# Performance work log

Measured on AMD Instinct MI355X. Metric: run time of the kernel, lower is better.

Reference implementation:

```python
import jax, jax.numpy as jnp
import numpy as np

B, D, MAXC = 16384, 64, 8
NPROB, NCON, TDIM, HID = 50000, 2000, 1024, 256

def setup_inputs() -> dict:
    key = jax.random.key(0)
    ks = jax.random.split(key, 20)
    s = 0.02
    return {
        'prob_ids': jax.random.randint(ks[0], (B,), 0, NPROB),
        'related_concept_index': jax.random.randint(ks[1], (B, MAXC), 0, NCON),
        'filter0': jax.random.randint(ks[2], (B, MAXC), 0, 2),
        'h': jax.random.normal(ks[3], (B, D), jnp.float32),
        'emb': jax.random.normal(ks[4], (B, 2 * D), jnp.float32),
        'operate': jax.random.randint(ks[5], (B, 1), 0, 2).astype(jnp.float32),
        'exercise_text_emb': jax.random.normal(ks[6], (NPROB, TDIM), jnp.float32) * s,
        'concept_text_emb': jax.random.normal(ks[7], (NCON, TDIM), jnp.float32) * s,
        'W1': jax.random.normal(ks[8], (TDIM, HID), jnp.float32) * s,
        'b1': jnp.zeros((HID,), jnp.float32),
        'W2': jax.random.normal(ks[9], (HID, D), jnp.float32) * s,
        'b2': jnp.zeros((D,), jnp.float32),
        'Wp': jax.random.normal(ks[10], (5 * D, 1), jnp.float32) * s,
        'bp': jnp.zeros((1,), jnp.float32),
        'Wx': jax.random.normal(ks[11], (4 * D, 3 * D), jnp.float32) * s,
        'Wh': jax.random.normal(ks[12], (D, 3 * D), jnp.float32) * s,
        'bx': jnp.zeros((3 * D,), jnp.float32),
        'bh': jnp.zeros((3 * D,), jnp.float32),
    }

def reference(prob_ids, related_concept_index, filter0, h, emb, operate,
              exercise_text_emb, concept_text_emb,
              W1, b1, W2, b2, Wp, bp, Wx, Wh, bx, bh):
    def text_proj(x):  # 1024 -> 256 -> 64 (dropout off at inference)
        return jax.nn.relu(x @ W1 + b1) @ W2 + b2

    red_prob = text_proj(exercise_text_emb)      # [NPROB, D]
    red_con = text_proj(concept_text_emb)        # [NCON, D]

    related = red_con[related_concept_index]     # gather: [B, MAXC, D]

    # text weights: cosine similarity of raw BERT embs (torch eps=1e-8)
    q = exercise_text_emb[prob_ids]              # [B, 1024]
    c = concept_text_emb[related_concept_index]  # [B, MAXC, 1024]
    dot = jnp.einsum('bd,bmd->bm', q, c)
    qn = jnp.sqrt(jnp.sum(q * q, axis=-1))[:, None]
    cn = jnp.sqrt(jnp.sum(c * c, axis=-1))
    tw = dot / jnp.maximum(qn * cn, 1e-8)
    tw = jnp.where(filter0 == 0, jnp.float32(-1e9), tw)
    tw = jax.nn.softmax(tw, axis=1)              # [B, MAXC]

    rep = jnp.einsum('bmd,bm->bd', related, tw)  # weighted concept sum
    v = jnp.concatenate([red_prob[prob_ids], rep], axis=1)  # [B, 2D]

    # predictor: funcs(n_layer=1, dim*5, 1) ~ single Linear
    prob = jnp.concatenate([h, v, emb], axis=1) @ Wp + bp   # [B, 1]

    # update_state -> GRU cell (mygru: input 4D, hidden D)
    op = operate
    v_cat = jnp.concatenate([v * op, v * (1 - op)], axis=1)
    e_cat = jnp.concatenate([emb * (1 - op), emb * op], axis=1)
    x = v_cat + e_cat                             # [B, 4D]
    xg = x @ Wx + bx
    hg = h @ Wh + bh
    xr, xz, xn = jnp.split(xg, 3, axis=1)
    hr, hz, hn = jnp.split(hg, 3, axis=1)
    r = jax.nn.sigmoid(xr + hr)
    z = jax.nn.sigmoid(xz + hz)
    n = jnp.tanh(xn + r * hn)
    h_next = (1 - z) * n + z * h                  # [B, D]
    return (prob, h_next)
```

## Files before the change

### kernel.cpp

```cpp
#include <hip/hip_runtime.h>
#include <cstdint>
#include <cstddef>

typedef unsigned short u16;
typedef unsigned char u8;
typedef long long i64;
typedef unsigned long long u64;
typedef __bf16 bf16x8 __attribute__((ext_vector_type(8)));
typedef float f32x4 __attribute__((ext_vector_type(4)));
typedef float f32x2 __attribute__((ext_vector_type(2)));
typedef u16 u16x4 __attribute__((ext_vector_type(4)));
typedef u16 u16x8 __attribute__((ext_vector_type(8)));

#define B_ 16384
#define D_ 64
#define MAXC_ 8
#define NCON_ 2000
#define NCONP_ 2048
#define TDIM_ 1024
#define HID_ 256

#define VMW(n) asm volatile("s_waitcnt vmcnt(" #n ")" ::: "memory")
#define BAR() __builtin_amdgcn_s_barrier()

__device__ inline u16 f2b(float f){
  unsigned u = __float_as_uint(f);
  u += 0x7fffu + ((u >> 16) & 1u);
  return (u16)(u >> 16);
}
__device__ inline float b2f(u16 u){ return __uint_as_float(((unsigned)u) << 16); }

__device__ inline unsigned pk2fp8(float a, float b){
  return (unsigned)__builtin_amdgcn_cvt_pk_fp8_f32(a, b, 0, false);
}

__device__ inline void gload16(const void* g, void* l){
  __builtin_amdgcn_global_load_lds((const __attribute__((address_space(1))) unsigned*)g,
                                   (__attribute__((address_space(3))) unsigned*)l, 16, 0, 0);
}

__device__ inline float wsum(float v){
  #pragma unroll
  for (int o = 32; o; o >>= 1) v += __shfl_xor(v, o);
  return v;
}
__device__ inline float sigf(float x){ return 1.f / (1.f + __expf(-x)); }

__global__ __launch_bounds__(256) void k_prep(
    const float* __restrict__ ex, const int* __restrict__ pid,
    const float* __restrict__ con,
    const float* __restrict__ W1, const float* __restrict__ W2,
    const float* __restrict__ Wx, const float* __restrict__ Wh,
    const float* __restrict__ bx, const float* __restrict__ bh,
    u8* __restrict__ qb8, float* __restrict__ qn,
    u8* __restrict__ cb8, float* __restrict__ cn,
    u8* __restrict__ W1T8, u16* __restrict__ W2T, u16* __restrict__ WxhT,
    float* __restrict__ bxh)
{
  const int bid = blockIdx.x, tid = threadIdx.x;
  const int lane = tid & 63;
  if (bid < 4096){
    const int b = bid * 4 + (tid >> 6);
    const float* src = ex + (size_t)pid[b] * TDIM_;
    u8* dst8 = qb8 + (size_t)b * TDIM_;
    float ss = 0.f;
    #pragma unroll
    for (int c = 0; c < 4; ++c){
      float4 v = *(const float4*)(src + c * 256 + lane * 4);
      ss += v.x*v.x + v.y*v.y + v.z*v.z + v.w*v.w;
      unsigned lo = pk2fp8(v.x * 32.f, v.y * 32.f);
      unsigned hi = pk2fp8(v.z * 32.f, v.w * 32.f);
      *(unsigned*)(dst8 + c * 256 + lane * 4) = (lo & 0xffffu) | (hi << 16);
    }
    ss = wsum(ss);
    if (lane == 0) qn[b] = sqrtf(ss);
  } else if (bid < 4608){
    const int r = (bid - 4096) * 4 + (tid >> 6);
    u8* dst8 = cb8 + (size_t)r * TDIM_;
    if (r < NCON_){
      const float* src = con + (size_t)r * TDIM_;
      float ss = 0.f;
      #pragma unroll
      for (int c = 0; c < 4; ++c){
        float4 v = *(const float4*)(src + c * 256 + lane * 4);
        ss += v.x*v.x + v.y*v.y + v.z*v.z + v.w*v.w;
        unsigned lo = pk2fp8(v.x * 32.f, v.y * 32.f);
        unsigned hi = pk2fp8(v.z * 32.f, v.w * 32.f);
        *(unsigned*)(dst8 + c * 256 + lane * 4) = (lo & 0xffffu) | (hi << 16);
      }
      ss = wsum(ss);
      if (lane == 0) cn[r] = sqrtf(ss);
    } else {
      #pragma unroll
      for (int c = 0; c < 4; ++c)
        *(unsigned*)(dst8 + c * 256 + lane * 4) = 0u;
    }
  } else {
    int gid = (bid - 4608) * 256 + tid;
    if (gid < 131072){
      int n = gid >> 9, k2 = (gid & 511) * 2;
      unsigned pk = pk2fp8(W1[(size_t)k2 * 256 + n] * 32.f,
                           W1[(size_t)(k2 + 1) * 256 + n] * 32.f);
      *(u16*)(W1T8 + (size_t)n * 1024 + k2) = (u16)pk;
    } else if (gid < 147456){
      int t = gid - 131072;
      int n = t >> 8, k = t & 255;
      W2T[t] = f2b(W2[(size_t)k * 64 + n]);
    } else if (gid < 229376){
      int t = gid - 147456;
      int c = t / 320, k = t % 320;
      int g = (c >> 4) & 3;
      int d = (c >> 6) * 16 + (c & 15);
      float v = 0.f;
      if (k < 256){
        if (g == 0)      v = Wx[(size_t)k * 192 + d];
        else if (g == 1) v = Wx[(size_t)k * 192 + 64 + d];
        else if (g == 2) v = Wx[(size_t)k * 192 + 128 + d];
      } else {
        int kh = k - 256;
        if (g == 0)      v = Wh[(size_t)kh * 192 + d];
        else if (g == 1) v = Wh[(size_t)kh * 192 + 64 + d];
        else if (g == 3) v = Wh[(size_t)kh * 192 + 128 + d];
      }
      WxhT[t] = f2b(v);
    } else if (gid < 229632){
      int c = gid - 229376;
      int g = (c >> 4) & 3;
      int d = (c >> 6) * 16 + (c & 15);
      float v;
      if (g == 0)      v = bx[d] + bh[d];
      else if (g == 1) v = bx[64 + d] + bh[64 + d];
      else if (g == 2) v = bx[128 + d];
      else             v = bh[128 + d];
      bxh[c] = v;
    }
  }
}

__global__ __launch_bounds__(512) void k_mlp(
    const u8* __restrict__ qb8, const u8* __restrict__ cb8,
    const u8* __restrict__ W1T8, const float* __restrict__ b1,
    const u16* __restrict__ W2T, const float* __restrict__ b2,
    float* __restrict__ redq, float* __restrict__ redc)
{
  __shared__ char SMm[53248];
  u16* Hs = (u16*)(SMm + 36864);
  const int tid = threadIdx.x;
  const int lane = tid & 63;
  const int w = tid >> 6;
  const int lr = lane & 15, lq = lane >> 4;
  const bool qside = blockIdx.x < 512;
  const u8* Abase = qside ? qb8 : cb8;
  float* Obase = qside ? redq : redc;
  const int m0 = (qside ? (int)blockIdx.x : ((int)blockIdx.x - 512)) << 5;
  const int rf = w & 1, ch = w >> 1;

  auto stage = [&](int buf, int kt){
    u8* Ab = (u8*)SMm + buf * 18432;
    u8* Bb = Ab + 2048;
    #pragma unroll
    for (int i = 0; i < 2; ++i){
      int e = i * 512 + tid;
      int slot = e >> 2, q4 = e & 3;
      int sw = (slot ^ (slot >> 2)) & 3;
      gload16(W1T8 + (size_t)slot * 1024 + kt * 64 + ((q4 ^ sw) << 4), Bb + e * 16);
    }
    if (tid < 128){
      int slot = tid >> 2, q4 = tid & 3;
      int sw = (slot ^ (slot >> 2)) & 3;
      gload16(Abase + (size_t)(m0 + slot) * TDIM_ + kt * 64 + ((q4 ^ sw) << 4),
              Ab + tid * 16);
    }
  };

  f32x4 acc[4] = {};
  stage(0, 0);
  int buf = 0;
  for (int kt = 0; kt < 16; ++kt){
    if (kt < 15){
      stage(buf ^ 1, kt + 1);
      if (w < 2) VMW(3); else VMW(2);
    } else VMW(0);
    BAR();
    const u8* Ab = (const u8*)SMm + buf * 18432;
    const u8* Bb = Ab + 2048;
    #pragma unroll
    for (int ks = 0; ks < 2; ++ks){
      const int h8 = ks * 4 + lq;
      const int arow = rf * 16 + lr;
      const int asw = (arow ^ (arow >> 2)) & 3;
      i64 a = *(const i64*)(Ab + arow * 64 + (((h8 >> 1) ^ asw) << 4) + (h8 & 1) * 8);
      #pragma unroll
      for (int fc = 0; fc < 4; ++fc){
        int brow = ch * 64 + fc * 16 + lr;
        int bsw = (brow ^ (brow >> 2)) & 3;
        i64 bv = *(const i64*)(Bb + brow * 64 + (((h8 >> 1) ^ bsw) << 4) + (h8 & 1) * 8);
        acc[fc] = __builtin_amdgcn_mfma_f32_16x16x32_fp8_fp8(a, bv, acc[fc], 0, 0, 0);
      }
    }
    BAR();
    buf ^= 1;
  }
  #pragma unroll
  for (int fc = 0; fc < 4; ++fc){
    int col = ch * 64 + fc * 16 + lr;
    float bv = b1[col];
    #pragma unroll
    for (int j = 0; j < 4; ++j){
      int rr = rf * 16 + lq * 4 + j;
      float v = fmaxf(acc[fc][j] * (1.f / 1024.f) + bv, 0.f);
      *(u16*)((char*)Hs + rr * 512 + ((col * 2) ^ ((rr & 7) << 4))) = f2b(v);
    }
  }
  __syncthreads();
  const int rf2 = w & 1, cp = w >> 1;
  f32x4 acc2 = {};
  #pragma unroll
  for (int ks2 = 0; ks2 < 8; ++ks2){
    int rr = rf2 * 16 + lr;
    int kb2 = ks2 * 64 + lq * 16;
    bf16x8 af2 = *(const bf16x8*)((const char*)Hs + rr * 512 + (kb2 ^ ((rr & 7) << 4)));
    bf16x8 w2 = *(const bf16x8*)(W2T + (size_t)(cp * 16 + lr) * 256 + ks2 * 32 + lq * 8);
    acc2 = __builtin_amdgcn_mfma_f32_16x16x32_bf16(af2, w2, acc2, 0, 0, 0);
  }
  {
    int col = cp * 16 + lr;
    float bv = b2[col];
    #pragma unroll
    for (int j = 0; j < 4; ++j){
      int rr = m0 + rf2 * 16 + lq * 4 + j;
      Obase[(size_t)rr * 64 + col] = acc2[j] + bv;
    }
  }
}

__global__ __launch_bounds__(512) void k_mixgru(
    const u8* __restrict__ qb8, const u8* __restrict__ cb8,
    const float* __restrict__ qn, const float* __restrict__ cn,
    const int* __restrict__ rci, const int* __restrict__ filt,
    const float* __restrict__ redq, const float* __restrict__ redc,
    const float* __restrict__ h, const float* __restrict__ emb,
    const float* __restrict__ op, const float* __restrict__ Wp,
    const float* __restrict__ bp, const u16* __restrict__ WxhT,
    const float* __restrict__ bxh, float* __restrict__ prob_out,
    float* __restrict__ outh)
{
  __shared__ char SM[67584];
  u8*    QsF  = (u8*)SM;
  u16*   XH   = (u16*)SM;
  float* DOTS = (float*)(SM + 20480);
  int*   SIDX = (int*)(SM + 32768);
  int*   SFLT = (int*)(SM + 33792);
  u8*    CsB  = (u8*)(SM + 34816);
  u16*   Bs   = (u16*)(SM + 34816);
  const int tid = threadIdx.x;
  const int lane = tid & 63;
  const int w = tid >> 6;
  const int m0 = blockIdx.x << 5;

  #pragma unroll
  for (int i = 0; i < 4; ++i){
    int e = i * 512 + tid;
    int row = e >> 6, c16 = e & 63;
    gload16(qb8 + (size_t)(m0 + row) * TDIM_ + ((c16 ^ (row & 7)) << 4),
            QsF + e * 16);
  }
  if (tid < 256) SIDX[tid] = rci[m0 * MAXC_ + tid];
  else           SFLT[tid - 256] = filt[m0 * MAXC_ + (tid - 256)];
  __syncthreads();

  auto stageC = [&](int buf, int kt){
    #pragma unroll
    for (int i = 0; i < 2; ++i){
      int e = i * 512 + tid;
      int slot = e >> 2, q4 = e & 3;
      int sw = (slot ^ (slot >> 2)) & 3;
      gload16(cb8 + (size_t)SIDX[slot] * TDIM_ + kt * 64 + ((q4 ^ sw) << 4),
              CsB + buf * 16384 + e * 16);
    }
  };

  const int R = w >> 2;
  const int cc0 = (w & 3) * 2;
  f32x4 dacc[2] = {};
  stageC(0, 0);
  int bufc = 0;
  for (int kt = 0; kt < 16; ++kt){
    if (kt < 15){ stageC(bufc ^ 1, kt + 1); VMW(2); }
    else        { VMW(0); }
    BAR();
    const u8* Cs = CsB + bufc * 16384;
    #pragma unroll
    for (int ks = 0; ks < 2; ++ks){
      const int h8 = ks * 4 + (lane >> 4);
      const int arow = R * 16 + (lane & 15);
      const int c16r = kt * 4 + (h8 >> 1);
      i64 a = *(const i64*)(QsF + arow * 1024 + ((c16r ^ (arow & 7)) << 4) + (h8 & 1) * 8);
      #pragma unroll
      for (int t = 0; t < 2; ++t){
        int slot = (R * 8 + cc0 + t) * 16 + (lane & 15);
        int bsw = (slot ^ (slot >> 2)) & 3;
        i64 bfr = *(const i64*)(Cs + slot * 64 + (((h8 >> 1) ^ bsw) << 4) + (h8 & 1) * 8);
        dacc[t] = __builtin_amdgcn_mfma_f32_16x16x32_fp8_fp8(a, bfr, dacc[t], 0, 0, 0);
      }
    }
    BAR();
    bufc ^= 1;
  }
  #pragma unroll
  for (int t = 0; t < 2; ++t){
    const int cc = cc0 + t;
    const int col = lane & 15;
    #pragma unroll
    for (int j = 0; j < 4; ++j){
      int tr = (lane >> 4) * 4 + j;
      if (tr == 2 * cc && col < 8)       DOTS[(R * 16 + tr) * 8 + col] = dacc[t][j];
      if (tr == 2 * cc + 1 && col >= 8)  DOTS[(R * 16 + tr) * 8 + col - 8] = dacc[t][j];
    }
  }
  auto stageB = [&](int kt){
    #pragma unroll
    for (int i = 0; i < 4; ++i){
      int cc = i * 512 + tid;
      int r2 = cc >> 3, s2 = cc & 7;
      gload16(WxhT + (size_t)r2 * 320 + kt * 64 + ((s2 ^ (r2 & 7)) << 3), &Bs[cc * 8]);
    }
  };
  __syncthreads();
  stageB(0);

  for (int i = 0; i < 4; ++i){
    const int r = w * 4 + i;
    const int b = m0 + r;
    int idxm[MAXC_];
    #pragma unroll
    for (int m = 0; m < MAXC_; ++m) idxm[m] = SIDX[r * MAXC_ + m];
    const float qnb = qn[b];
    float sv[MAXC_]; float mx = -3.0e38f;
    #pragma unroll
    for (int m = 0; m < MAXC_; ++m){
      float dnm = fmaxf(qnb * cn[idxm[m]], 1e-8f);
      float s = (SFLT[r * MAXC_ + m] == 0) ? -1e9f
              : DOTS[r * 8 + m] * (1.f / 1024.f) / dnm;
      sv[m] = s; mx = fmaxf(mx, s);
    }
    float se = 0.f;
    #pragma unroll
    for (int m = 0; m < MAXC_; ++m){ sv[m] = __expf(sv[m] - mx); se += sv[m]; }
    const float inv = 1.f / se;
    float rep = 0.f;
    #pragma unroll
    for (int m = 0; m < MAXC_; ++m) rep += sv[m] * redc[(size_t)idxm[m] * D_ + lane];
    rep *= inv;
    const float v0 = redq[(size_t)b * D_ + lane];
    const float hv = h[(size_t)b * D_ + lane];
    const float e0 = emb[(size_t)b * 128 + lane];
    const float e1 = emb[(size_t)b * 128 + 64 + lane];
    float p = hv * Wp[lane] + v0 * Wp[64 + lane] + rep * Wp[128 + lane]
            + e0 * Wp[192 + lane] + e1 * Wp[256 + lane];
    p = wsum(p);
    if (lane == 0) prob_out[b] = p + bp[0];
    const float o = op[b], om = 1.f - o;
    auto xst = [&](int col, float v){
      *(u16*)((char*)XH + r * 640 + ((col * 2) ^ ((r & 7) << 4))) = f2b(v);
    };
    xst(lane,        v0 * o  + e0 * om);
    xst(64 + lane,   rep * o + e1 * om);
    xst(128 + lane,  v0 * om + e0 * o);
    xst(192 + lane,  rep * om + e1 * o);
    xst(256 + lane,  hv);
  }
  __syncthreads();

  const int lr = lane & 15, lq = lane >> 4;
  const int rh = w & 1, cc2 = w >> 1;
  f32x4 acc[4] = {};
  for (int kt = 0; kt < 5; ++kt){
    VMW(0);
    BAR();
    #pragma unroll
    for (int ks = 0; ks < 2; ++ks){
      const int kb = ks * 64 + lq * 16;
      int rra = rh * 16 + lr;
      bf16x8 af = *(const bf16x8*)((const char*)XH + rra * 640 +
                                   ((kt * 128 + kb) ^ ((rra & 7) << 4)));
      bf16x8 bfr[4];
      #pragma unroll
      for (int fc = 0; fc < 4; ++fc){
        int rr = cc2 * 64 + fc * 16 + lr;
        bfr[fc] = *(const bf16x8*)((const char*)Bs + rr * 128 + (kb ^ ((rr & 7) << 4)));
      }
      #pragma unroll
      for (int fc = 0; fc < 4; ++fc)
        acc[fc] = __builtin_amdgcn_mfma_f32_16x16x32_bf16(af, bfr[fc], acc[fc], 0, 0, 0);
    }
    BAR();
    if (kt < 4) stageB(kt + 1);
  }
  const int d = cc2 * 16 + lr;
  float bg[4];
  #pragma unroll
  for (int g = 0; g < 4; ++g) bg[g] = bxh[cc2 * 64 + g * 16 + lr];
  #pragma unroll
  for (int j = 0; j < 4; ++j){
    float rv = sigf(acc[0][j] + bg[0]);
    float zv = sigf(acc[1][j] + bg[1]);
    float nv = tanhf(acc[2][j] + bg[2] + rv * (acc[3][j] + bg[3]));
    int rr = m0 + rh * 16 + lq * 4 + j;
    float hv = h[(size_t)rr * 64 + d];
    outh[(size_t)rr * 64 + d] = (1.f - zv) * nv + zv * hv;
  }
}

extern "C" void kernel_launch(void* const* d_in, const int* in_sizes, int n_in,
                              void* d_out, int out_size, void* d_ws, size_t ws_size,
                              hipStream_t stream) {
  const int*   prob_ids = (const int*)  d_in[0];
  const int*   rci      = (const int*)  d_in[1];
  const int*   filt     = (const int*)  d_in[2];
  const float* h        = (const float*)d_in[3];
  const float* emb      = (const float*)d_in[4];
  const float* op       = (const float*)d_in[5];
  const float* ex       = (const float*)d_in[6];
  const float* con      = (const float*)d_in[7];
  const float* W1       = (const float*)d_in[8];
  const float* b1       = (const float*)d_in[9];
  const float* W2       = (const float*)d_in[10];
  const float* b2       = (const float*)d_in[11];
  const float* Wp       = (const float*)d_in[12];
  const float* bp       = (const float*)d_in[13];
  const float* Wx       = (const float*)d_in[14];
  const float* Wh       = (const float*)d_in[15];
  const float* bx       = (const float*)d_in[16];
  const float* bh       = (const float*)d_in[17];
  float* out = (float*)d_out;

  char* w = (char*)d_ws;
  size_t off = 0;
  auto alloc = [&](size_t bytes){ size_t o = off; off = (off + bytes + 255) & ~(size_t)255; return o; };
  u8*    qb8  = (u8*)   (w + alloc((size_t)B_ * TDIM_));
  u8*    cb8  = (u8*)   (w + alloc((size_t)NCONP_ * TDIM_));
  float* qn   = (float*)(w + alloc((size_t)B_ * 4));
  float* cn   = (float*)(w + alloc((size_t)NCONP_ * 4));
  float* redq = (float*)(w + alloc((size_t)B_ * D_ * 4));
  float* redc = (float*)(w + alloc((size_t)NCONP_ * D_ * 4));
  u8*    W1T8 = (u8*)   (w + alloc((size_t)HID_ * TDIM_));
  u16*   W2T  = (u16*)  (w + alloc((size_t)D_ * HID_ * 2));
  u16*   WxhT = (u16*)  (w + alloc((size_t)256 * 320 * 2));
  float* bxh  = (float*)(w + alloc((size_t)256 * 4));

  k_prep<<<5505, 256, 0, stream>>>(ex, prob_ids, con, W1, W2, Wx, Wh, bx, bh,
                                   qb8, qn, cb8, cn, W1T8, W2T, WxhT, bxh);
  k_mlp<<<576, 512, 0, stream>>>(qb8, cb8, W1T8, b1, W2T, b2, redq, redc);
  k_mixgru<<<512, 512, 0, stream>>>(qb8, cb8, qn, cn, rci, filt, redq, redc,
                                    h, emb, op, Wp, bp, WxhT, bxh, out, out + B_);
}
```

Before: 71.59 us.

## Fuse query-side text MLP into mix/GRU kernel, keep projection in LDS

The query-side 1024->256->64 projection moves out of the separate MLP kernel and into the mix/GRU kernel. It reuses the query fp8 tile already staged in shared memory and keeps the reduced vector in LDS instead of writing it to global memory and reading it back. The MLP kernel now handles only the concept table with 64 blocks. This removes one global round trip of the query projection and its separate reload of the query rows, at the cost of a longer fused kernel with more shared memory and a serialized W1 phase before the cosine/dot phase.

```diff
diff --git a/kernel.cpp b/kernel.cpp
--- a/kernel.cpp
+++ b/kernel.cpp
@@ -9,7 +9,6 @@
 typedef __bf16 bf16x8 __attribute__((ext_vector_type(8)));
 typedef float f32x4 __attribute__((ext_vector_type(4)));
 typedef float f32x2 __attribute__((ext_vector_type(2)));
-typedef u16 u16x4 __attribute__((ext_vector_type(4)));
 typedef u16 u16x8 __attribute__((ext_vector_type(8)));
 
 #define B_ 16384
@@ -137,11 +136,11 @@
   }
 }
 
-__global__ __launch_bounds__(512) void k_mlp(
-    const u8* __restrict__ qb8, const u8* __restrict__ cb8,
+__global__ __launch_bounds__(512) void k_cmlp(
+    const u8* __restrict__ cb8,
     const u8* __restrict__ W1T8, const float* __restrict__ b1,
     const u16* __restrict__ W2T, const float* __restrict__ b2,
-    float* __restrict__ redq, float* __restrict__ redc)
+    float* __restrict__ redc)
 {
   __shared__ char SMm[53248];
   u16* Hs = (u16*)(SMm + 36864);
@@ -149,10 +148,7 @@
   const int lane = tid & 63;
   const int w = tid >> 6;
   const int lr = lane & 15, lq = lane >> 4;
-  const bool qside = blockIdx.x < 512;
-  const u8* Abase = qside ? qb8 : cb8;
-  float* Obase = qside ? redq : redc;
-  const int m0 = (qside ? (int)blockIdx.x : ((int)blockIdx.x - 512)) << 5;
+  const int m0 = (int)blockIdx.x << 5;
   const int rf = w & 1, ch = w >> 1;
 
   auto stage = [&](int buf, int kt){
@@ -168,7 +164,7 @@
     if (tid < 128){
       int slot = tid >> 2, q4 = tid & 3;
       int sw = (slot ^ (slot >> 2)) & 3;
-      gload16(Abase + (size_t)(m0 + slot) * TDIM_ + kt * 64 + ((q4 ^ sw) << 4),
+      gload16(cb8 + (size_t)(m0 + slot) * TDIM_ + kt * 64 + ((q4 ^ sw) << 4),
               Ab + tid * 16);
     }
   };
@@ -229,33 +225,37 @@
     #pragma unroll
     for (int j = 0; j < 4; ++j){
       int rr = m0 + rf2 * 16 + lq * 4 + j;
-      Obase[(size_t)rr * 64 + col] = acc2[j] + bv;
-    }
-  }
-}
-
-__global__ __launch_bounds__(512) void k_mixgru(
+      redc[(size_t)rr * 64 + col] = acc2[j] + bv;
+    }
+  }
+}
+
+__global__ __launch_bounds__(512, 4) void k_fused(
     const u8* __restrict__ qb8, const u8* __restrict__ cb8,
     const float* __restrict__ qn, const float* __restrict__ cn,
     const int* __restrict__ rci, const int* __restrict__ filt,
-    const float* __restrict__ redq, const float* __restrict__ redc,
+    const float* __restrict__ redc,
     const float* __restrict__ h, const float* __restrict__ emb,
     const float* __restrict__ op, const float* __restrict__ Wp,
-    const float* __restrict__ bp, const u16* __restrict__ WxhT,
-    const float* __restrict__ bxh, float* __restrict__ prob_out,
-    float* __restrict__ outh)
+    const float* __restrict__ bp,
+    const u8* __restrict__ W1T8, const float* __restrict__ b1,
+    const u16* __restrict__ W2T, const float* __restrict__ b2,
+    const u16* __restrict__ WxhT, const float* __restrict__ bxh,
+    float* __restrict__ prob_out, float* __restrict__ outh)
 {
-  __shared__ char SM[67584];
+  __shared__ char SM[75776];
   u8*    QsF  = (u8*)SM;
   u16*   XH   = (u16*)SM;
   float* DOTS = (float*)(SM + 20480);
-  int*   SIDX = (int*)(SM + 32768);
-  int*   SFLT = (int*)(SM + 33792);
-  u8*    CsB  = (u8*)(SM + 34816);
-  u16*   Bs   = (u16*)(SM + 34816);
+  u16*   Hs   = (u16*)(SM + 32768);
+  u16*   Bs   = (u16*)(SM + 32768);
+  float* Rq   = (float*)(SM + 65536);
+  int*   SIDX = (int*)(SM + 73728);
+  int*   SFLT = (int*)(SM + 74752);
   const int tid = threadIdx.x;
   const int lane = tid & 63;
   const int w = tid >> 6;
+  const int lr = lane & 15, lq = lane >> 4;
   const int m0 = blockIdx.x << 5;
 
   #pragma unroll
@@ -265,47 +265,120 @@
     gload16(qb8 + (size_t)(m0 + row) * TDIM_ + ((c16 ^ (row & 7)) << 4),
             QsF + e * 16);
   }
-  if (tid < 256) SIDX[tid] = rci[m0 * MAXC_ + tid];
-  else           SFLT[tid - 256] = filt[m0 * MAXC_ + (tid - 256)];
-  __syncthreads();
-
+  int rv;
+  if (tid < 256) rv = rci[m0 * MAXC_ + tid];
+  else           rv = filt[m0 * MAXC_ + (tid - 256)];
+
+  auto stageW1 = [&](int buf, int kt){
+    u8* Bb = (u8*)SM + 32768 + buf * 16384;
+    #pragma unroll
+    for (int i = 0; i < 2; ++i){
+      int e = i * 512 + tid;
+      int slot = e >> 2, q4 = e & 3;
+      int sw = (slot ^ (slot >> 2)) & 3;
+      gload16(W1T8 + (size_t)slot * 1024 + kt * 64 + ((q4 ^ sw) << 4), Bb + e * 16);
+    }
+  };
   auto stageC = [&](int buf, int kt){
+    u8* Bb = (u8*)SM + 32768 + buf * 16384;
     #pragma unroll
     for (int i = 0; i < 2; ++i){
       int e = i * 512 + tid;
       int slot = e >> 2, q4 = e & 3;
       int sw = (slot ^ (slot >> 2)) & 3;
       gload16(cb8 + (size_t)SIDX[slot] * TDIM_ + kt * 64 + ((q4 ^ sw) << 4),
-              CsB + buf * 16384 + e * 16);
+              Bb + e * 16);
     }
   };
+
+  const int rf = w & 1, ch = w >> 1;
+  f32x4 acc[4] = {};
+  stageW1(0, 0);
+  int buf = 0;
+  for (int kt = 0; kt < 16; ++kt){
+    if (kt < 15){ stageW1(buf ^ 1, kt + 1); VMW(2); }
+    else        { VMW(0); }
+    BAR();
+    const u8* Bb = (const u8*)SM + 32768 + buf * 16384;
+    #pragma unroll
+    for (int ks = 0; ks < 2; ++ks){
+      const int h8 = ks * 4 + lq;
+      const int arow = rf * 16 + lr;
+      const int c16r = kt * 4 + (h8 >> 1);
+      i64 a = *(const i64*)(QsF + arow * 1024 + ((c16r ^ (arow & 7)) << 4) + (h8 & 1) * 8);
+      #pragma unroll
+      for (int fc = 0; fc < 4; ++fc){
+        int brow = ch * 64 + fc * 16 + lr;
+        int bsw = (brow ^ (brow >> 2)) & 3;
+        i64 bv = *(const i64*)(Bb + brow * 64 + (((h8 >> 1) ^ bsw) << 4) + (h8 & 1) * 8);
+        acc[fc] = __builtin_amdgcn_mfma_f32_16x16x32_fp8_fp8(a, bv, acc[fc], 0, 0, 0);
+      }
+    }
+    BAR();
+    buf ^= 1;
+  }
+  #pragma unroll
+  for (int fc = 0; fc < 4; ++fc){
+    int col = ch * 64 + fc * 16 + lr;
+    float bv = b1[col];
+    #pragma unroll
+    for (int j = 0; j < 4; ++j){
+      int rr = rf * 16 + lq * 4 + j;
+      float v = fmaxf(acc[fc][j] * (1.f / 1024.f) + bv, 0.f);
+      *(u16*)((char*)Hs + rr * 512 + ((col * 2) ^ ((rr & 7) << 4))) = f2b(v);
+    }
+  }
+  if (tid < 256) SIDX[tid] = rv;
+  else           SFLT[tid - 256] = rv;
+  __syncthreads();
+
+  stageC(1, 0);
+  {
+    const int rf2 = w & 1, cp = w >> 1;
+    f32x4 acc2 = {};
+    #pragma unroll
+    for (int ks2 = 0; ks2 < 8; ++ks2){
+      int rr = rf2 * 16 + lr;
+      int kb2 = ks2 * 64 + lq * 16;
+      bf16x8 af2 = *(const bf16x8*)((const char*)Hs + rr * 512 + (kb2 ^ ((rr & 7) << 4)));
+      bf16x8 w2 = *(const bf16x8*)(W2T + (size_t)(cp * 16 + lr) * 256 + ks2 * 32 + lq * 8);
+      acc2 = __builtin_amdgcn_mfma_f32_16x16x32_bf16(af2, w2, acc2, 0, 0, 0);
+    }
+    int col = cp * 16 + lr;
+    float bv = b2[col];
+    #pragma unroll
+    for (int j = 0; j < 4; ++j){
+      int rr = rf2 * 16 + lq * 4 + j;
+      Rq[rr * 64 + col] = acc2[j] + bv;
+    }
+  }
+  __syncthreads();
 
   const int R = w >> 2;
   const int cc0 = (w & 3) * 2;
   f32x4 dacc[2] = {};
-  stageC(0, 0);
-  int bufc = 0;
+  int bufd = 1;
   for (int kt = 0; kt < 16; ++kt){
-    if (kt < 15){ stageC(bufc ^ 1, kt + 1); VMW(2); }
+    if (kt < 15){ stageC(bufd ^ 1, kt + 1); VMW(2); }
     else        { VMW(0); }
     BAR();
-    const u8* Cs = CsB + bufc * 16384;
+    const u8* Cs = (const u8*)SM + 32768 + bufd * 16384;
     #pragma unroll
     for (int ks = 0; ks < 2; ++ks){
-      const int h8 = ks * 4 + (lane >> 4);
-      const int arow = R * 16 + (lane & 15);
+      const int h8 = ks * 4 + lq;
+      const int arow = R * 16 + lr;
       const int c16r = kt * 4 + (h8 >> 1);
       i64 a = *(const i64*)(QsF + arow * 1024 + ((c16r ^ (arow & 7)) << 4) + (h8 & 1) * 8);
       #pragma unroll
       for (int t = 0; t < 2; ++t){
-        int slot = (R * 8 + cc0 + t) * 16 + (lane & 15);
+        int slot = (R * 8 + cc0 + t) * 16 + lr;
         int bsw = (slot ^ (slot >> 2)) & 3;
         i64 bfr = *(const i64*)(Cs + slot * 64 + (((h8 >> 1) ^ bsw) << 4) + (h8 & 1) * 8);
         dacc[t] = __builtin_amdgcn_mfma_f32_16x16x32_fp8_fp8(a, bfr, dacc[t], 0, 0, 0);
       }
     }
     BAR();
-    bufc ^= 1;
+    bufd ^= 1;
   }
   #pragma unroll
   for (int t = 0; t < 2; ++t){
@@ -313,7 +386,7 @@
     const int col = lane & 15;
     #pragma unroll
     for (int j = 0; j < 4; ++j){
-      int tr = (lane >> 4) * 4 + j;
+      int tr = lq * 4 + j;
       if (tr == 2 * cc && col < 8)       DOTS[(R * 16 + tr) * 8 + col] = dacc[t][j];
       if (tr == 2 * cc + 1 && col >= 8)  DOTS[(R * 16 + tr) * 8 + col - 8] = dacc[t][j];
     }
@@ -352,7 +425,7 @@
     #pragma unroll
     for (int m = 0; m < MAXC_; ++m) rep += sv[m] * redc[(size_t)idxm[m] * D_ + lane];
     rep *= inv;
-    const float v0 = redq[(size_t)b * D_ + lane];
+    const float v0 = Rq[r * 64 + lane];
     const float hv = h[(size_t)b * D_ + lane];
     const float e0 = emb[(size_t)b * 128 + lane];
     const float e1 = emb[(size_t)b * 128 + 64 + lane];
@@ -372,9 +445,8 @@
   }
   __syncthreads();
 
-  const int lr = lane & 15, lq = lane >> 4;
   const int rh = w & 1, cc2 = w >> 1;
-  f32x4 acc[4] = {};
+  f32x4 gacc[4] = {};
   for (int kt = 0; kt < 5; ++kt){
     VMW(0);
     BAR();
@@ -392,7 +464,7 @@
       }
       #pragma unroll
       for (int fc = 0; fc < 4; ++fc)
-        acc[fc] = __builtin_amdgcn_mfma_f32_16x16x32_bf16(af, bfr[fc], acc[fc], 0, 0, 0);
+        gacc[fc] = __builtin_amdgcn_mfma_f32_16x16x32_bf16(af, bfr[fc], gacc[fc], 0, 0, 0);
     }
     BAR();
     if (kt < 4) stageB(kt + 1);
@@ -403,9 +475,9 @@
   for (int g = 0; g < 4; ++g) bg[g] = bxh[cc2 * 64 + g * 16 + lr];
   #pragma unroll
   for (int j = 0; j < 4; ++j){
-    float rv = sigf(acc[0][j] + bg[0]);
-    float zv = sigf(acc[1][j] + bg[1]);
-    float nv = tanhf(acc[2][j] + bg[2] + rv * (acc[3][j] + bg[3]));
+    float rvv = sigf(gacc[0][j] + bg[0]);
+    float zv = sigf(gacc[1][j] + bg[1]);
+    float nv = tanhf(gacc[2][j] + bg[2] + rvv * (gacc[3][j] + bg[3]));
     int rr = m0 + rh * 16 + lq * 4 + j;
     float hv = h[(size_t)rr * 64 + d];
     outh[(size_t)rr * 64 + d] = (1.f - zv) * nv + zv * hv;
@@ -442,7 +514,6 @@
   u8*    cb8  = (u8*)   (w + alloc((size_t)NCONP_ * TDIM_));
   float* qn   = (float*)(w + alloc((size_t)B_ * 4));
   float* cn   = (float*)(w + alloc((size_t)NCONP_ * 4));
-  float* redq = (float*)(w + alloc((size_t)B_ * D_ * 4));
   float* redc = (float*)(w + alloc((size_t)NCONP_ * D_ * 4));
   u8*    W1T8 = (u8*)   (w + alloc((size_t)HID_ * TDIM_));
   u16*   W2T  = (u16*)  (w + alloc((size_t)D_ * HID_ * 2));
@@ -451,7 +522,8 @@
 
   k_prep<<<5505, 256, 0, stream>>>(ex, prob_ids, con, W1, W2, Wx, Wh, bx, bh,
                                    qb8, qn, cb8, cn, W1T8, W2T, WxhT, bxh);
-  k_mlp<<<576, 512, 0, stream>>>(qb8, cb8, W1T8, b1, W2T, b2, redq, redc);
-  k_mixgru<<<512, 512, 0, stream>>>(qb8, cb8, qn, cn, rci, filt, redq, redc,
-                                    h, emb, op, Wp, bp, WxhT, bxh, out, out + B_);
-}
+  k_cmlp<<<64, 512, 0, stream>>>(cb8, W1T8, b1, W2T, b2, redc);
+  k_fused<<<512, 512, 0, stream>>>(qb8, cb8, qn, cn, rci, filt, redc,
+                                   h, emb, op, Wp, bp,
+                                   W1T8, b1, W2T, b2, WxhT, bxh, out, out + B_);
+}
```

Measured after the change: 72.15 us. About the same (+0.8%).

## Compute cosine text weights in query-prep kernel using fp32 query and fp8 concepts

Applied to the files above, without the earlier changes.

Splits the prep kernel into a concept/weight prep kernel and a query prep kernel. The query kernel now also computes the dot products against the gathered fp8 concept rows, using the fp32 query values already in registers, and writes the softmaxed text weights to a buffer. This removes the fp8 MFMA dot-product stage, its LDS staging and the qn buffer from the GRU kernel, which then just reads the weights. The cost is an extra kernel launch, a serial dependency of query prep on concept prep, and scalar gathered loads in place of MFMA for the dots.

```diff
diff --git a/kernel.cpp b/kernel.cpp
--- a/kernel.cpp
+++ b/kernel.cpp
@@ -9,7 +9,6 @@
 typedef __bf16 bf16x8 __attribute__((ext_vector_type(8)));
 typedef float f32x4 __attribute__((ext_vector_type(4)));
 typedef float f32x2 __attribute__((ext_vector_type(2)));
-typedef u16 u16x4 __attribute__((ext_vector_type(4)));
 typedef u16 u16x8 __attribute__((ext_vector_type(8)));
 
 #define B_ 16384
@@ -33,6 +32,10 @@
 __device__ inline unsigned pk2fp8(float a, float b){
   return (unsigned)__builtin_amdgcn_cvt_pk_fp8_f32(a, b, 0, false);
 }
+template<bool HI>
+__device__ inline f32x2 unpk_fp8(unsigned v){
+  return __builtin_amdgcn_cvt_pk_f32_fp8(v, HI);
+}
 
 __device__ inline void gload16(const void* g, void* l){
   __builtin_amdgcn_global_load_lds((const __attribute__((address_space(1))) unsigned*)g,
@@ -46,36 +49,19 @@
 }
 __device__ inline float sigf(float x){ return 1.f / (1.f + __expf(-x)); }
 
-__global__ __launch_bounds__(256) void k_prep(
-    const float* __restrict__ ex, const int* __restrict__ pid,
+__global__ __launch_bounds__(256) void k_prepc(
     const float* __restrict__ con,
     const float* __restrict__ W1, const float* __restrict__ W2,
     const float* __restrict__ Wx, const float* __restrict__ Wh,
     const float* __restrict__ bx, const float* __restrict__ bh,
-    u8* __restrict__ qb8, float* __restrict__ qn,
     u8* __restrict__ cb8, float* __restrict__ cn,
     u8* __restrict__ W1T8, u16* __restrict__ W2T, u16* __restrict__ WxhT,
     float* __restrict__ bxh)
 {
   const int bid = blockIdx.x, tid = threadIdx.x;
   const int lane = tid & 63;
-  if (bid < 4096){
-    const int b = bid * 4 + (tid >> 6);
-    const float* src = ex + (size_t)pid[b] * TDIM_;
-    u8* dst8 = qb8 + (size_t)b * TDIM_;
-    float ss = 0.f;
-    #pragma unroll
-    for (int c = 0; c < 4; ++c){
-      float4 v = *(const float4*)(src + c * 256 + lane * 4);
-      ss += v.x*v.x + v.y*v.y + v.z*v.z + v.w*v.w;
-      unsigned lo = pk2fp8(v.x * 32.f, v.y * 32.f);
-      unsigned hi = pk2fp8(v.z * 32.f, v.w * 32.f);
-      *(unsigned*)(dst8 + c * 256 + lane * 4) = (lo & 0xffffu) | (hi << 16);
-    }
-    ss = wsum(ss);
-    if (lane == 0) qn[b] = sqrtf(ss);
-  } else if (bid < 4608){
-    const int r = (bid - 4096) * 4 + (tid >> 6);
+  if (bid < 512){
+    const int r = bid * 4 + (tid >> 6);
     u8* dst8 = cb8 + (size_t)r * TDIM_;
     if (r < NCON_){
       const float* src = con + (size_t)r * TDIM_;
@@ -96,7 +82,7 @@
         *(unsigned*)(dst8 + c * 256 + lane * 4) = 0u;
     }
   } else {
-    int gid = (bid - 4608) * 256 + tid;
+    int gid = (bid - 512) * 256 + tid;
     if (gid < 131072){
       int n = gid >> 9, k2 = (gid & 511) * 2;
       unsigned pk = pk2fp8(W1[(size_t)k2 * 256 + n] * 32.f,
@@ -137,6 +123,83 @@
   }
 }
 
+__global__ __launch_bounds__(256) void k_prepq(
+    const float* __restrict__ ex, const int* __restrict__ pid,
+    const u8* __restrict__ cb8, const float* __restrict__ cn,
+    const int* __restrict__ rci, const int* __restrict__ filt,
+    u8* __restrict__ qb8, float* __restrict__ tw)
+{
+  const int tid = threadIdx.x;
+  const int lane = tid & 63;
+  const int b = blockIdx.x * 4 + (tid >> 6);
+  const float* src = ex + (size_t)pid[b] * TDIM_;
+  u8* dst8 = qb8 + (size_t)b * TDIM_;
+
+  float4 v0 = *(const float4*)(src + 0 * 256 + lane * 4);
+  float4 v1 = *(const float4*)(src + 1 * 256 + lane * 4);
+  float4 v2 = *(const float4*)(src + 2 * 256 + lane * 4);
+  float4 v3 = *(const float4*)(src + 3 * 256 + lane * 4);
+  int idxm[MAXC_];
+  #pragma unroll
+  for (int m = 0; m < MAXC_; ++m) idxm[m] = rci[b * MAXC_ + m];
+
+  float ss = v0.x*v0.x + v0.y*v0.y + v0.z*v0.z + v0.w*v0.w
+           + v1.x*v1.x + v1.y*v1.y + v1.z*v1.z + v1.w*v1.w
+           + v2.x*v2.x + v2.y*v2.y + v2.z*v2.z + v2.w*v2.w
+           + v3.x*v3.x + v3.y*v3.y + v3.z*v3.z + v3.w*v3.w;
+  {
+    unsigned w0 = (pk2fp8(v0.x*32.f, v0.y*32.f) & 0xffffu) | (pk2fp8(v0.z*32.f, v0.w*32.f) << 16);
+    unsigned w1 = (pk2fp8(v1.x*32.f, v1.y*32.f) & 0xffffu) | (pk2fp8(v1.z*32.f, v1.w*32.f) << 16);
+    unsigned w2 = (pk2fp8(v2.x*32.f, v2.y*32.f) & 0xffffu) | (pk2fp8(v2.z*32.f, v2.w*32.f) << 16);
+    unsigned w3 = (pk2fp8(v3.x*32.f, v3.y*32.f) & 0xffffu) | (pk2fp8(v3.z*32.f, v3.w*32.f) << 16);
+    *(unsigned*)(dst8 + 0 * 256 + lane * 4) = w0;
+    *(unsigned*)(dst8 + 1 * 256 + lane * 4) = w1;
+    *(unsigned*)(dst8 + 2 * 256 + lane * 4) = w2;
+    *(unsigned*)(dst8 + 3 * 256 + lane * 4) = w3;
+  }
+
+  float dots[MAXC_];
+  #pragma unroll
+  for (int m = 0; m < MAXC_; ++m){
+    const u8* crow = cb8 + (size_t)idxm[m] * TDIM_ + lane * 4;
+    unsigned c0 = *(const unsigned*)(crow);
+    unsigned c1 = *(const unsigned*)(crow + 256);
+    unsigned c2 = *(const unsigned*)(crow + 512);
+    unsigned c3 = *(const unsigned*)(crow + 768);
+    float s = 0.f; f32x2 p;
+    p = unpk_fp8<false>(c0); s += v0.x*p[0] + v0.y*p[1];
+    p = unpk_fp8<true >(c0); s += v0.z*p[0] + v0.w*p[1];
+    p = unpk_fp8<false>(c1); s += v1.x*p[0] + v1.y*p[1];
+    p = unpk_fp8<true >(c1); s += v1.z*p[0] + v1.w*p[1];
+    p = unpk_fp8<false>(c2); s += v2.x*p[0] + v2.y*p[1];
+    p = unpk_fp8<true >(c2); s += v2.z*p[0] + v2.w*p[1];
+    p = unpk_fp8<false>(c3); s += v3.x*p[0] + v3.y*p[1];
+    p = unpk_fp8<true >(c3); s += v3.z*p[0] + v3.w*p[1];
+    dots[m] = s;
+  }
+  #pragma unroll
+  for (int o = 32; o; o >>= 1){
+    #pragma unroll
+    for (int m = 0; m < MAXC_; ++m) dots[m] += __shfl_xor(dots[m], o);
+    ss += __shfl_xor(ss, o);
+  }
+  const float qnb = sqrtf(ss);
+  float sv[MAXC_]; float mx = -3.0e38f;
+  #pragma unroll
+  for (int m = 0; m < MAXC_; ++m){
+    float dnm = fmaxf(qnb * cn[idxm[m]], 1e-8f);
+    float s = (filt[b * MAXC_ + m] == 0) ? -1e9f : dots[m] * (1.f / 32.f) / dnm;
+    sv[m] = s; mx = fmaxf(mx, s);
+  }
+  float se = 0.f;
+  #pragma unroll
+  for (int m = 0; m < MAXC_; ++m){ sv[m] = __expf(sv[m] - mx); se += sv[m]; }
+  const float inv = 1.f / se;
+  #pragma unroll
+  for (int m = 0; m < MAXC_; ++m)
+    if (lane == m) tw[(size_t)b * MAXC_ + m] = sv[m] * inv;
+}
+
 __global__ __launch_bounds__(512) void k_mlp(
     const u8* __restrict__ qb8, const u8* __restrict__ cb8,
     const u8* __restrict__ W1T8, const float* __restrict__ b1,
@@ -235,9 +298,7 @@
 }
 
 __global__ __launch_bounds__(512) void k_mixgru(
-    const u8* __restrict__ qb8, const u8* __restrict__ cb8,
-    const float* __restrict__ qn, const float* __restrict__ cn,
-    const int* __restrict__ rci, const int* __restrict__ filt,
+    const float* __restrict__ tw, const int* __restrict__ rci,
     const float* __restrict__ redq, const float* __restrict__ redc,
     const float* __restrict__ h, const float* __restrict__ emb,
     const float* __restrict__ op, const float* __restrict__ Wp,
@@ -245,79 +306,15 @@
     const float* __restrict__ bxh, float* __restrict__ prob_out,
     float* __restrict__ outh)
 {
-  __shared__ char SM[67584];
-  u8*    QsF  = (u8*)SM;
-  u16*   XH   = (u16*)SM;
-  float* DOTS = (float*)(SM + 20480);
-  int*   SIDX = (int*)(SM + 32768);
-  int*   SFLT = (int*)(SM + 33792);
-  u8*    CsB  = (u8*)(SM + 34816);
-  u16*   Bs   = (u16*)(SM + 34816);
+  __shared__ char SM[54272];
+  u16* XH   = (u16*)SM;
+  int* SIDX = (int*)(SM + 20480);
+  u16* Bs   = (u16*)(SM + 21504);
   const int tid = threadIdx.x;
   const int lane = tid & 63;
   const int w = tid >> 6;
   const int m0 = blockIdx.x << 5;
 
-  #pragma unroll
-  for (int i = 0; i < 4; ++i){
-    int e = i * 512 + tid;
-    int row = e >> 6, c16 = e & 63;
-    gload16(qb8 + (size_t)(m0 + row) * TDIM_ + ((c16 ^ (row & 7)) << 4),
-            QsF + e * 16);
-  }
-  if (tid < 256) SIDX[tid] = rci[m0 * MAXC_ + tid];
-  else           SFLT[tid - 256] = filt[m0 * MAXC_ + (tid - 256)];
-  __syncthreads();
-
-  auto stageC = [&](int buf, int kt){
-    #pragma unroll
-    for (int i = 0; i < 2; ++i){
-      int e = i * 512 + tid;
-      int slot = e >> 2, q4 = e & 3;
-      int sw = (slot ^ (slot >> 2)) & 3;
-      gload16(cb8 + (size_t)SIDX[slot] * TDIM_ + kt * 64 + ((q4 ^ sw) << 4),
-              CsB + buf * 16384 + e * 16);
-    }
-  };
-
-  const int R = w >> 2;
-  const int cc0 = (w & 3) * 2;
-  f32x4 dacc[2] = {};
-  stageC(0, 0);
-  int bufc = 0;
-  for (int kt = 0; kt < 16; ++kt){
-    if (kt < 15){ stageC(bufc ^ 1, kt + 1); VMW(2); }
-    else        { VMW(0); }
-    BAR();
-    const u8* Cs = CsB + bufc * 16384;
-    #pragma unroll
-    for (int ks = 0; ks < 2; ++ks){
-      const int h8 = ks * 4 + (lane >> 4);
-      const int arow = R * 16 + (lane & 15);
-      const int c16r = kt * 4 + (h8 >> 1);
-      i64 a = *(const i64*)(QsF + arow * 1024 + ((c16r ^ (arow & 7)) << 4) + (h8 & 1) * 8);
-      #pragma unroll
-      for (int t = 0; t < 2; ++t){
-        int slot = (R * 8 + cc0 + t) * 16 + (lane & 15);
-        int bsw = (slot ^ (slot >> 2)) & 3;
-        i64 bfr = *(const i64*)(Cs + slot * 64 + (((h8 >> 1) ^ bsw) << 4) + (h8 & 1) * 8);
-        dacc[t] = __builtin_amdgcn_mfma_f32_16x16x32_fp8_fp8(a, bfr, dacc[t], 0, 0, 0);
-      }
-    }
-    BAR();
-    bufc ^= 1;
-  }
-  #pragma unroll
-  for (int t = 0; t < 2; ++t){
-    const int cc = cc0 + t;
-    const int col = lane & 15;
-    #pragma unroll
-    for (int j = 0; j < 4; ++j){
-      int tr = (lane >> 4) * 4 + j;
-      if (tr == 2 * cc && col < 8)       DOTS[(R * 16 + tr) * 8 + col] = dacc[t][j];
-      if (tr == 2 * cc + 1 && col >= 8)  DOTS[(R * 16 + tr) * 8 + col - 8] = dacc[t][j];
-    }
-  }
   auto stageB = [&](int kt){
     #pragma unroll
     for (int i = 0; i < 4; ++i){
@@ -326,8 +323,9 @@
       gload16(WxhT + (size_t)r2 * 320 + kt * 64 + ((s2 ^ (r2 & 7)) << 3), &Bs[cc * 8]);
     }
   };
+  if (tid < 256) SIDX[tid] = rci[m0 * MAXC_ + tid];
+  stageB(0);
   __syncthreads();
-  stageB(0);
 
   for (int i = 0; i < 4; ++i){
     const int r = w * 4 + i;
@@ -335,23 +333,12 @@
     int idxm[MAXC_];
     #pragma unroll
     for (int m = 0; m < MAXC_; ++m) idxm[m] = SIDX[r * MAXC_ + m];
-    const float qnb = qn[b];
-    float sv[MAXC_]; float mx = -3.0e38f;
-    #pragma unroll
-    for (int m = 0; m < MAXC_; ++m){
-      float dnm = fmaxf(qnb * cn[idxm[m]], 1e-8f);
-      float s = (SFLT[r * MAXC_ + m] == 0) ? -1e9f
-              : DOTS[r * 8 + m] * (1.f / 1024.f) / dnm;
-      sv[m] = s; mx = fmaxf(mx, s);
-    }
-    float se = 0.f;
-    #pragma unroll
-    for (int m = 0; m < MAXC_; ++m){ sv[m] = __expf(sv[m] - mx); se += sv[m]; }
-    const float inv = 1.f / se;
+    float twv[MAXC_];
+    #pragma unroll
+    for (int m = 0; m < MAXC_; ++m) twv[m] = tw[(size_t)b * MAXC_ + m];
     float rep = 0.f;
     #pragma unroll
-    for (int m = 0; m < MAXC_; ++m) rep += sv[m] * redc[(size_t)idxm[m] * D_ + lane];
-    rep *= inv;
+    for (int m = 0; m < MAXC_; ++m) rep += twv[m] * redc[(size_t)idxm[m] * D_ + lane];
     const float v0 = redq[(size_t)b * D_ + lane];
     const float hv = h[(size_t)b * D_ + lane];
     const float e0 = emb[(size_t)b * 128 + lane];
@@ -440,8 +427,8 @@
   auto alloc = [&](size_t bytes){ size_t o = off; off = (off + bytes + 255) & ~(size_t)255; return o; };
   u8*    qb8  = (u8*)   (w + alloc((size_t)B_ * TDIM_));
   u8*    cb8  = (u8*)   (w + alloc((size_t)NCONP_ * TDIM_));
-  float* qn   = (float*)(w + alloc((size_t)B_ * 4));
   float* cn   = (float*)(w + alloc((size_t)NCONP_ * 4));
+  float* tw   = (float*)(w + alloc((size_t)B_ * MAXC_ * 4));
   float* redq = (float*)(w + alloc((size_t)B_ * D_ * 4));
   float* redc = (float*)(w + alloc((size_t)NCONP_ * D_ * 4));
   u8*    W1T8 = (u8*)   (w + alloc((size_t)HID_ * TDIM_));
@@ -449,9 +436,10 @@
   u16*   WxhT = (u16*)  (w + alloc((size_t)256 * 320 * 2));
   float* bxh  = (float*)(w + alloc((size_t)256 * 4));
 
-  k_prep<<<5505, 256, 0, stream>>>(ex, prob_ids, con, W1, W2, Wx, Wh, bx, bh,
-                                   qb8, qn, cb8, cn, W1T8, W2T, WxhT, bxh);
+  k_prepc<<<1409, 256, 0, stream>>>(con, W1, W2, Wx, Wh, bx, bh,
+                                    cb8, cn, W1T8, W2T, WxhT, bxh);
+  k_prepq<<<4096, 256, 0, stream>>>(ex, prob_ids, cb8, cn, rci, filt, qb8, tw);
   k_mlp<<<576, 512, 0, stream>>>(qb8, cb8, W1T8, b1, W2T, b2, redq, redc);
-  k_mixgru<<<512, 512, 0, stream>>>(qb8, cb8, qn, cn, rci, filt, redq, redc,
-                                    h, emb, op, Wp, bp, WxhT, bxh, out, out + B_);
-}
+  k_mixgru<<<512, 512, 0, stream>>>(tw, rci, redq, redc, h, emb, op, Wp, bp,
+                                    WxhT, bxh, out, out + B_);
+}
```

Result: slower. 75.17 us (+5.0%).
